# Kernel tuning notes

Measured on AMD Instinct MI355X. Metric: run time of the kernel, lower is better.

The kernel has to match this reference:

```python
import jax, jax.numpy as jnp
import numpy as np

N_NODES = 100000
IN_CH, HIDDEN, OUT_CH = 128, 64, 40
N_EDGES = 1600000


def gcn_conv(x, row, col, W, b, num_nodes):
    """PyG GCNConv: x' = D^-1/2 (A+I) D^-1/2 (x W) + b, self-loops already in row/col."""
    h = x @ W  # [N, out]
    deg = jax.ops.segment_sum(jnp.ones_like(col, dtype=h.dtype), col, num_segments=num_nodes)
    dinv = jnp.where(deg > 0, jax.lax.rsqrt(deg), 0.0)  # [N]
    norm = dinv[row] * dinv[col]  # [E+N]
    msg = h[row] * norm[:, None]  # gather + scale
    out = jax.ops.segment_sum(msg, col, num_segments=num_nodes)  # scatter-add to targets
    return out + b


def setup_inputs() -> dict:
    key = jax.random.key(0)
    k = jax.random.split(key, 6)
    x = jax.random.normal(k[0], (N_NODES, IN_CH), dtype=jnp.float32)
    ei = jax.random.randint(k[1], (2, N_EDGES), 0, N_NODES, dtype=jnp.int64)
    # Glorot-style init for linear weights, zeros for biases (PyG defaults)
    W1 = jax.random.normal(k[2], (IN_CH, HIDDEN), dtype=jnp.float32) / np.sqrt(IN_CH)
    b1 = jnp.zeros((HIDDEN,), dtype=jnp.float32)
    W2 = jax.random.normal(k[3], (HIDDEN, OUT_CH), dtype=jnp.float32) / np.sqrt(HIDDEN)
    b2 = jnp.zeros((OUT_CH,), dtype=jnp.float32)
    return {"x": x, "ei": ei, "W1": W1, "b1": b1, "W2": W2, "b2": b2}


def reference(x, ei, W1, b1, W2, b2):
    num_nodes = x.shape[0]
    loop = jnp.arange(num_nodes, dtype=ei.dtype)
    row = jnp.concatenate([ei[0], loop])  # sources + self-loops
    col = jnp.concatenate([ei[1], loop])  # targets + self-loops
    h = jax.nn.relu(gcn_conv(x, row, col, W1, b1, num_nodes))
    # dropout(p=0.5) is identity in eval mode (deterministic reference)
    return gcn_conv(h, row, col, W2, b2, num_nodes)
```

## Files before the change

### kernel.cpp

```cpp
#include <hip/hip_runtime.h>
#include <hip/hip_bf16.h>
#include <math.h>

#define IN_CH 128
#define HID 64
#define OUT_CH 40
#define NBUCK 1024
#define NBSHIFT 10
#define CAP2 3125
#define CAPL 2560

typedef const __hip_bfloat16* bf16p;
typedef __attribute__((ext_vector_type(8))) short bf16x8;
typedef __attribute__((ext_vector_type(4))) float f32x4;
typedef __attribute__((ext_vector_type(8))) float f32x8;

__device__ __forceinline__ f32x8 cvt8(bf16x8 v) {
    f32x8 o;
    #pragma unroll
    for (int j = 0; j < 8; ++j) {
        unsigned int bits = ((unsigned int)(unsigned short)v[j]) << 16;
        o[j] = __uint_as_float(bits);
    }
    return o;
}

__device__ __forceinline__ bf16x8 pack8(f32x8 v) {
    bf16x8 o;
    #pragma unroll
    for (int j = 0; j < 8; ++j) {
        __hip_bfloat16 b = __float2bfloat16(v[j]);
        o[j] = *reinterpret_cast<short*>(&b);
    }
    return o;
}

__device__ __forceinline__ int bucket_of(int c, int N, float invNB) {
    int b = (int)((float)c * invNB);
    long long cB = (long long)c << NBSHIFT;
    while ((long long)(b + 1) * N <= cB) ++b;
    while (b > 0 && (long long)b * N > cB) --b;
    return b;
}

__global__ __launch_bounds__(256) void k_detectconv(const void* x, const void* ei,
        int* flags, const void* W1, const void* b1, const void* W2, const void* b2,
        float* wf, int* bincnt2) {
    __shared__ int s_f32, s_hi;
    if (threadIdx.x == 0) { s_f32 = 0; s_hi = 0; }
    __syncthreads();
    const __hip_bfloat16* xb = (const __hip_bfloat16*)x;
    const int* ii = (const int*)ei;
    int lf = 0, lh = 0;
    for (int i = threadIdx.x; i < 4096; i += 256) {
        float f = __bfloat162float(xb[i]);
        if (!(fabsf(f) <= 1e4f)) lf = 1;
        lh |= ii[2 * i + 1];
    }
    if (lf) atomicOr(&s_f32, 1);
    if (lh) atomicOr(&s_hi, 1);
    for (int i = threadIdx.x; i < NBUCK; i += 256) bincnt2[i] = 0;
    __syncthreads();
    const int isF32 = s_f32 ? 1 : 0;
    if (threadIdx.x == 0) {
        flags[0] = isF32;
        flags[1] = (s_hi == 0) ? 1 : 0;
        flags[2] = 0;
    }
    for (int i = threadIdx.x; i < 10856; i += 256) {
        const void* src; int off;
        if (i < 8192)       { src = W1; off = i; }
        else if (i < 8256)  { src = b1; off = i - 8192; }
        else if (i < 10816) { src = W2; off = i - 8256; }
        else                { src = b2; off = i - 10816; }
        wf[i] = isF32 ? ((const float*)src)[off]
                      : __bfloat162float(((bf16p)src)[off]);
    }
}

__global__ __launch_bounds__(512) void k_bin2(const int* ei, const int* flags,
        int* bincnt2, long long* bins2, int E, int N, float invNB) {
    __shared__ int cnt[NBUCK], base[NBUCK];
    for (int i = threadIdx.x; i < NBUCK; i += 512) cnt[i] = 0;
    __syncthreads();
    const int i64 = flags[1];
    const int e0 = blockIdx.x * 4096;
    const int e1 = min(e0 + 4096, E);
    int e = e0 + threadIdx.x;
    for (; e + 3 * 512 < e1; e += 4 * 512) {
        int c0 = i64 ? ei[2 * (E + e)]        : ei[E + e];
        int c1 = i64 ? ei[2 * (E + e + 512)]  : ei[E + e + 512];
        int c2 = i64 ? ei[2 * (E + e + 1024)] : ei[E + e + 1024];
        int c3 = i64 ? ei[2 * (E + e + 1536)] : ei[E + e + 1536];
        atomicAdd(&cnt[bucket_of(c0, N, invNB)], 1);
        atomicAdd(&cnt[bucket_of(c1, N, invNB)], 1);
        atomicAdd(&cnt[bucket_of(c2, N, invNB)], 1);
        atomicAdd(&cnt[bucket_of(c3, N, invNB)], 1);
    }
    for (; e < e1; e += 512) {
        int c = i64 ? ei[2 * (E + e)] : ei[E + e];
        atomicAdd(&cnt[bucket_of(c, N, invNB)], 1);
    }
    __syncthreads();
    for (int i = threadIdx.x; i < NBUCK; i += 512) {
        int v = cnt[i];
        base[i] = v ? atomicAdd(&bincnt2[i], v) : 0;
        cnt[i] = 0;
    }
    __syncthreads();
    for (e = e0 + threadIdx.x; e < e1; e += 512) {
        int r, c;
        if (i64) { r = ei[2 * e]; c = ei[2 * (E + e)]; }
        else     { r = ei[e];     c = ei[E + e]; }
        int b = bucket_of(c, N, invNB);
        int slot = base[b] + atomicAdd(&cnt[b], 1);
        if (slot < CAP2)
            bins2[(size_t)b * CAP2 + slot] = ((long long)r << 32) | (unsigned int)c;
    }
}

__global__ __launch_bounds__(256) void k_csr(const long long* bins2, const int* bincnt2,
        int* rowstart, float* dinv, int* erow, int N) {
    __shared__ long long rc[CAPL];
    __shared__ int sdeg[256], lcur[256], red[256];
    const int s = blockIdx.x;
    const int tid = threadIdx.x;
    int part = 0;
    for (int j = tid; j < s; j += 256) part += min(bincnt2[j], CAPL);
    red[tid] = part;
    __syncthreads();
    for (int o = 128; o > 0; o >>= 1) {
        if (tid < o) red[tid] += red[tid + o];
        __syncthreads();
    }
    const int gb = red[0];
    const int nlo = (int)(((long long)s * N + NBUCK - 1) >> NBSHIFT);
    const int nhi = (int)(((long long)(s + 1) * N + NBUCK - 1) >> NBSHIFT);
    const int width = nhi - nlo;
    const int cnt = min(bincnt2[s], CAPL);

    for (int i = tid; i < cnt; i += 256) rc[i] = bins2[(size_t)s * CAP2 + i];
    sdeg[tid] = 0;
    __syncthreads();
    for (int i = tid; i < cnt; i += 256) {
        int j = (int)(rc[i] & 0xffffffffLL) - nlo;
        if (j >= 0 && j < width) atomicAdd(&sdeg[j], 1);
    }
    __syncthreads();
    int my = sdeg[tid];
    __syncthreads();
    for (int off = 1; off < 256; off <<= 1) {
        int t = (tid >= off) ? sdeg[tid - off] : 0;
        __syncthreads();
        sdeg[tid] += t;
        __syncthreads();
    }
    int excl = sdeg[tid] - my;
    lcur[tid] = excl;
    if (tid < width) {
        rowstart[nlo + tid] = gb + excl;
        dinv[nlo + tid] = rsqrtf((float)my + 1.0f);
    }
    if (s == NBUCK - 1 && tid == 0) rowstart[N] = gb + cnt;
    __syncthreads();
    for (int i = tid; i < cnt; i += 256) {
        long long v = rc[i];
        int j = (int)(v & 0xffffffffLL) - nlo;
        if (j >= 0 && j < width) {
            int pos = atomicAdd(&lcur[j], 1);
            erow[gb + pos] = (int)(v >> 32);
        }
    }
}

__global__ __launch_bounds__(256) void k_gemm1_mfma(const void* x, const float* W1f,
        __hip_bfloat16* h1b, const int* flags, int N) {
    __shared__ __align__(16) unsigned short wT[HID][IN_CH];
    for (int i = threadIdx.x; i < IN_CH * HID; i += 256) {
        int k = i >> 6, c = i & 63;
        __hip_bfloat16 b = __float2bfloat16(W1f[i]);
        wT[c][k] = *reinterpret_cast<unsigned short*>(&b);
    }
    __syncthreads();

    const int isF32 = flags[0];
    const int lane = threadIdx.x & 63;
    const int wid  = threadIdx.x >> 6;
    const int r = lane & 15;
    const int g = lane >> 4;

    bf16x8 bfr[4][4];
    #pragma unroll
    for (int nt = 0; nt < 4; ++nt)
        #pragma unroll
        for (int ks = 0; ks < 4; ++ks)
            bfr[nt][ks] = *(const bf16x8*)&wT[nt * 16 + r][ks * 32 + g * 8];

    const int tiles = (N + 15) >> 4;
    for (int t = blockIdx.x * 4 + wid; t < tiles; t += gridDim.x * 4) {
        const int row0 = t * 16;
        int arow = row0 + r; if (arow >= N) arow = N - 1;
        bf16x8 afr[4];
        if (!isF32) {
            const unsigned short* xr = (const unsigned short*)x + (size_t)arow * IN_CH;
            #pragma unroll
            for (int ks = 0; ks < 4; ++ks)
                afr[ks] = *(const bf16x8*)&xr[ks * 32 + g * 8];
        } else {
            const float* xr = (const float*)x + (size_t)arow * IN_CH;
            #pragma unroll
            for (int ks = 0; ks < 4; ++ks) {
                f32x4 a0 = *(const f32x4*)&xr[ks * 32 + g * 8];
                f32x4 a1 = *(const f32x4*)&xr[ks * 32 + g * 8 + 4];
                #pragma unroll
                for (int j = 0; j < 4; ++j) {
                    __hip_bfloat16 b0 = __float2bfloat16(a0[j]);
                    __hip_bfloat16 b1v = __float2bfloat16(a1[j]);
                    afr[ks][j]     = *reinterpret_cast<short*>(&b0);
                    afr[ks][j + 4] = *reinterpret_cast<short*>(&b1v);
                }
            }
        }
        f32x4 acc[4] = {};
        #pragma unroll
        for (int ks = 0; ks < 4; ++ks)
            #pragma unroll
            for (int nt = 0; nt < 4; ++nt)
                acc[nt] = __builtin_amdgcn_mfma_f32_16x16x32_bf16(afr[ks], bfr[nt][ks],
                                                                  acc[nt], 0, 0, 0);
        #pragma unroll
        for (int nt = 0; nt < 4; ++nt) {
            #pragma unroll
            for (int q = 0; q < 4; ++q) {
                int rr = row0 + g * 4 + q;
                if (rr < N)
                    h1b[(size_t)rr * HID + nt * 16 + r] = __float2bfloat16(acc[nt][q]);
            }
        }
    }
}

__global__ __launch_bounds__(256) void k_agg1(const int* rowstart, const int* erow,
        const __hip_bfloat16* h1b, const float* dinv, const float* b1f,
        __hip_bfloat16* g, int N) {
    const int lane = threadIdx.x & 63;
    const int sub = lane >> 3;
    const int co  = lane & 7;
    const f32x4 b1a = *(const f32x4*)&b1f[co * 8];
    const f32x4 b1b = *(const f32x4*)&b1f[co * 8 + 4];
    const int wstride = (gridDim.x * 256) >> 6;
    for (int w = (blockIdx.x * 256 + threadIdx.x) >> 6; w < N; w += wstride) {
        int s0 = __builtin_amdgcn_readfirstlane(rowstart[w]);
        int s1 = __builtin_amdgcn_readfirstlane(rowstart[w + 1]);
        float d = dinv[w];
        bf16x8 sv = *(const bf16x8*)&h1b[(size_t)w * HID + co * 8];
        f32x8 acc = {};
        int i = s0 + sub;
        for (; i + 8 < s1; i += 16) {
            int r0 = erow[i], r1 = erow[i + 8];
            float n0 = dinv[r0] * d, n1 = dinv[r1] * d;
            f32x8 v0 = cvt8(*(const bf16x8*)&h1b[(size_t)r0 * HID + co * 8]);
            f32x8 v1 = cvt8(*(const bf16x8*)&h1b[(size_t)r1 * HID + co * 8]);
            #pragma unroll
            for (int j = 0; j < 8; ++j) {
                acc[j] = fmaf(v0[j], n0, acc[j]);
                acc[j] = fmaf(v1[j], n1, acc[j]);
            }
        }
        if (i < s1) {
            int r0 = erow[i];
            float n0 = dinv[r0] * d;
            f32x8 v0 = cvt8(*(const bf16x8*)&h1b[(size_t)r0 * HID + co * 8]);
            #pragma unroll
            for (int j = 0; j < 8; ++j) acc[j] = fmaf(v0[j], n0, acc[j]);
        }
        #pragma unroll
        for (int j = 0; j < 8; ++j) {
            acc[j] += __shfl_xor(acc[j], 8);
            acc[j] += __shfl_xor(acc[j], 16);
            acc[j] += __shfl_xor(acc[j], 32);
        }
        if (sub == 0) {
            float dd = d * d;
            f32x8 sf = cvt8(sv);
            f32x8 gv;
            #pragma unroll
            for (int j = 0; j < 4; ++j) {
                gv[j]     = fmaxf(fmaf(sf[j], dd, acc[j]) + b1a[j], 0.f);
                gv[j + 4] = fmaxf(fmaf(sf[j + 4], dd, acc[j + 4]) + b1b[j], 0.f);
            }
            *(bf16x8*)&g[(size_t)w * HID + co * 8] = pack8(gv);
        }
    }
}

__global__ __launch_bounds__(256) void k_agg2s(const int* rowstart, const int* erow,
        const __hip_bfloat16* g, const float* dinv, __hip_bfloat16* sbuf, int N) {
    const int lane = threadIdx.x & 63;
    const int sub = lane >> 3;
    const int co  = lane & 7;
    const int wstride = (gridDim.x * 256) >> 6;
    for (int w = (blockIdx.x * 256 + threadIdx.x) >> 6; w < N; w += wstride) {
        int s0 = __builtin_amdgcn_readfirstlane(rowstart[w]);
        int s1 = __builtin_amdgcn_readfirstlane(rowstart[w + 1]);
        float d = dinv[w];
        bf16x8 sv = *(const bf16x8*)&g[(size_t)w * HID + co * 8];
        f32x8 acc = {};
        int i = s0 + sub;
        for (; i + 8 < s1; i += 16) {
            int r0 = erow[i], r1 = erow[i + 8];
            float n0 = dinv[r0] * d, n1 = dinv[r1] * d;
            f32x8 v0 = cvt8(*(const bf16x8*)&g[(size_t)r0 * HID + co * 8]);
            f32x8 v1 = cvt8(*(const bf16x8*)&g[(size_t)r1 * HID + co * 8]);
            #pragma unroll
            for (int j = 0; j < 8; ++j) {
                acc[j] = fmaf(v0[j], n0, acc[j]);
                acc[j] = fmaf(v1[j], n1, acc[j]);
            }
        }
        if (i < s1) {
            int r0 = erow[i];
            float n0 = dinv[r0] * d;
            f32x8 v0 = cvt8(*(const bf16x8*)&g[(size_t)r0 * HID + co * 8]);
            #pragma unroll
            for (int j = 0; j < 8; ++j) acc[j] = fmaf(v0[j], n0, acc[j]);
        }
        #pragma unroll
        for (int j = 0; j < 8; ++j) {
            acc[j] += __shfl_xor(acc[j], 8);
            acc[j] += __shfl_xor(acc[j], 16);
            acc[j] += __shfl_xor(acc[j], 32);
        }
        if (sub == 0) {
            float dd = d * d;
            f32x8 sf = cvt8(sv);
            f32x8 ov;
            #pragma unroll
            for (int j = 0; j < 8; ++j) ov[j] = fmaf(sf[j], dd, acc[j]);
            *(bf16x8*)&sbuf[(size_t)w * HID + co * 8] = pack8(ov);
        }
    }
}

__global__ __launch_bounds__(256) void k_gemm2_mfma(const __hip_bfloat16* sbuf,
        const float* W2f, const float* b2f, float* out, int N) {
    __shared__ __align__(16) unsigned short w2T[48][HID];
    for (int i = threadIdx.x; i < 48 * HID; i += 256) {
        int c = i >> 6, k = i & 63;
        float v = (c < OUT_CH) ? W2f[k * OUT_CH + c] : 0.f;
        __hip_bfloat16 b = __float2bfloat16(v);
        w2T[c][k] = *reinterpret_cast<unsigned short*>(&b);
    }
    __syncthreads();

    const int lane = threadIdx.x & 63;
    const int wid  = threadIdx.x >> 6;
    const int r = lane & 15;
    const int gq = lane >> 4;

    bf16x8 bfr[3][2];
    #pragma unroll
    for (int nt = 0; nt < 3; ++nt)
        #pragma unroll
        for (int ks = 0; ks < 2; ++ks)
            bfr[nt][ks] = *(const bf16x8*)&w2T[nt * 16 + r][ks * 32 + gq * 8];
    float b2v[3];
    #pragma unroll
    for (int nt = 0; nt < 3; ++nt)
        b2v[nt] = (nt * 16 + r < OUT_CH) ? b2f[nt * 16 + r] : 0.f;

    const int tiles = (N + 15) >> 4;
    for (int t = blockIdx.x * 4 + wid; t < tiles; t += gridDim.x * 4) {
        const int row0 = t * 16;
        int arow = row0 + r; if (arow >= N) arow = N - 1;
        const unsigned short* sr = (const unsigned short*)sbuf + (size_t)arow * HID;
        bf16x8 afr[2];
        afr[0] = *(const bf16x8*)&sr[gq * 8];
        afr[1] = *(const bf16x8*)&sr[32 + gq * 8];
        f32x4 acc[3] = {};
        #pragma unroll
        for (int ks = 0; ks < 2; ++ks)
            #pragma unroll
            for (int nt = 0; nt < 3; ++nt)
                acc[nt] = __builtin_amdgcn_mfma_f32_16x16x32_bf16(afr[ks], bfr[nt][ks],
                                                                  acc[nt], 0, 0, 0);
        #pragma unroll
        for (int nt = 0; nt < 3; ++nt) {
            int c = nt * 16 + r;
            #pragma unroll
            for (int q = 0; q < 4; ++q) {
                int rr = row0 + gq * 4 + q;
                if (rr < N && c < OUT_CH)
                    out[(size_t)rr * OUT_CH + c] = acc[nt][q] + b2v[nt];
            }
        }
    }
}

extern "C" void kernel_launch(void* const* d_in, const int* in_sizes, int n_in,
                              void* d_out, int out_size, void* d_ws, size_t ws_size,
                              hipStream_t stream) {
    const void* x  = d_in[0];
    const void* ei = d_in[1];
    const void* W1 = d_in[2];
    const void* b1 = d_in[3];
    const void* W2 = d_in[4];
    const void* b2 = d_in[5];
    const int N = in_sizes[0] / IN_CH;
    const int E = in_sizes[1] / 2;
    const int* eii = (const int*)ei;

    float* ws = (float*)d_ws;
    size_t off = 16;
    int*   flags    = (int*)ws;
    int*   bincnt2  = (int*)ws + off;            off += NBUCK;
    float* dinv     = ws + off;                  off += N;
    float* wf       = ws + off;                  off += 10880;
    int*   rowstart = (int*)ws + off;            off += N + 1;
    off = (off + 255) & ~(size_t)255;
    int*   erow     = (int*)ws + off;            off += E;
    off = (off + 255) & ~(size_t)255;
    __hip_bfloat16* h1b = (__hip_bfloat16*)(ws + off);     off += (size_t)N * HID / 2;
    __hip_bfloat16* g   = (__hip_bfloat16*)(ws + off);     off += (size_t)N * HID / 2;
    __hip_bfloat16* sbuf = h1b;
    long long* bins2 = (long long*)h1b;

    k_detectconv<<<1, 256, 0, stream>>>(x, ei, flags, W1, b1, W2, b2, wf, bincnt2);

    float invNB = (float)NBUCK / (float)N;
    int nbin = (E + 4095) / 4096;
    k_bin2<<<nbin, 512, 0, stream>>>(eii, flags, bincnt2, bins2, E, N, invNB);
    k_csr<<<NBUCK, 256, 0, stream>>>(bins2, bincnt2, rowstart, dinv, erow, N);

    int tiles = (N + 15) / 16;
    int g1 = (tiles + 7) / 8;
    k_gemm1_mfma<<<g1, 256, 0, stream>>>(x, wf, h1b, flags, N);

    k_agg1<<<4096, 256, 0, stream>>>(rowstart, erow, h1b, dinv, wf + 8192, g, N);
    k_agg2s<<<4096, 256, 0, stream>>>(rowstart, erow, g, dinv, sbuf, N);
    k_gemm2_mfma<<<g1, 256, 0, stream>>>(sbuf, wf + 8256, wf + 10816, (float*)d_out, N);
}
```

Baseline: 270.9 us.

## Pre-scale features by dinv and pack edge bins into 32-bit words

The symmetric normalization is folded into the features. GEMM1 output is multiplied by dinv[src], and the layer-1 output is multiplied by dinv again before storage, so both aggregation kernels become plain sums with no per-edge dinv gather or multiply. The edge bins also shrink from 64-bit (row,col) pairs to 32-bit words holding the row shifted left by 7 and the column offset within the bucket, which halves binning traffic and shared memory in k_csr. The packing assumes node ids fit in 25 bits and bucket widths are at most 128, and pre-scaling rounds to bf16 at a different point.

```diff
diff --git a/kernel.cpp b/kernel.cpp
--- a/kernel.cpp
+++ b/kernel.cpp
@@ -79,7 +79,7 @@
 }
 
 __global__ __launch_bounds__(512) void k_bin2(const int* ei, const int* flags,
-        int* bincnt2, long long* bins2, int E, int N, float invNB) {
+        int* bincnt2, unsigned int* bins2, int E, int N, float invNB) {
     __shared__ int cnt[NBUCK], base[NBUCK];
     for (int i = threadIdx.x; i < NBUCK; i += 512) cnt[i] = 0;
     __syncthreads();
@@ -113,15 +113,17 @@
         if (i64) { r = ei[2 * e]; c = ei[2 * (E + e)]; }
         else     { r = ei[e];     c = ei[E + e]; }
         int b = bucket_of(c, N, invNB);
+        int nlo = (int)(((long long)b * N + NBUCK - 1) >> NBSHIFT);
         int slot = base[b] + atomicAdd(&cnt[b], 1);
         if (slot < CAP2)
-            bins2[(size_t)b * CAP2 + slot] = ((long long)r << 32) | (unsigned int)c;
-    }
-}
-
-__global__ __launch_bounds__(256) void k_csr(const long long* bins2, const int* bincnt2,
+            bins2[(size_t)b * CAP2 + slot] =
+                ((unsigned int)r << 7) | (unsigned int)(c - nlo);
+    }
+}
+
+__global__ __launch_bounds__(256) void k_csr(const unsigned int* bins2, const int* bincnt2,
         int* rowstart, float* dinv, int* erow, int N) {
-    __shared__ long long rc[CAPL];
+    __shared__ unsigned int rc[CAPL];
     __shared__ int sdeg[256], lcur[256], red[256];
     const int s = blockIdx.x;
     const int tid = threadIdx.x;
@@ -143,8 +145,8 @@
     sdeg[tid] = 0;
     __syncthreads();
     for (int i = tid; i < cnt; i += 256) {
-        int j = (int)(rc[i] & 0xffffffffLL) - nlo;
-        if (j >= 0 && j < width) atomicAdd(&sdeg[j], 1);
+        int j = (int)(rc[i] & 127u);
+        if (j < width) atomicAdd(&sdeg[j], 1);
     }
     __syncthreads();
     int my = sdeg[tid];
@@ -164,17 +166,17 @@
     if (s == NBUCK - 1 && tid == 0) rowstart[N] = gb + cnt;
     __syncthreads();
     for (int i = tid; i < cnt; i += 256) {
-        long long v = rc[i];
-        int j = (int)(v & 0xffffffffLL) - nlo;
-        if (j >= 0 && j < width) {
+        unsigned int v = rc[i];
+        int j = (int)(v & 127u);
+        if (j < width) {
             int pos = atomicAdd(&lcur[j], 1);
-            erow[gb + pos] = (int)(v >> 32);
+            erow[gb + pos] = (int)(v >> 7);
         }
     }
 }
 
 __global__ __launch_bounds__(256) void k_gemm1_mfma(const void* x, const float* W1f,
-        __hip_bfloat16* h1b, const int* flags, int N) {
+        const float* dinv, __hip_bfloat16* h1s, const int* flags, int N) {
     __shared__ __align__(16) unsigned short wT[HID][IN_CH];
     for (int i = threadIdx.x; i < IN_CH * HID; i += 256) {
         int k = i >> 6, c = i & 63;
@@ -229,20 +231,22 @@
                 acc[nt] = __builtin_amdgcn_mfma_f32_16x16x32_bf16(afr[ks], bfr[nt][ks],
                                                                   acc[nt], 0, 0, 0);
         #pragma unroll
-        for (int nt = 0; nt < 4; ++nt) {
-            #pragma unroll
-            for (int q = 0; q < 4; ++q) {
-                int rr = row0 + g * 4 + q;
-                if (rr < N)
-                    h1b[(size_t)rr * HID + nt * 16 + r] = __float2bfloat16(acc[nt][q]);
+        for (int q = 0; q < 4; ++q) {
+            int rr = row0 + g * 4 + q;
+            if (rr < N) {
+                float dv = dinv[rr];
+                #pragma unroll
+                for (int nt = 0; nt < 4; ++nt)
+                    h1s[(size_t)rr * HID + nt * 16 + r] =
+                        __float2bfloat16(acc[nt][q] * dv);
             }
         }
     }
 }
 
 __global__ __launch_bounds__(256) void k_agg1(const int* rowstart, const int* erow,
-        const __hip_bfloat16* h1b, const float* dinv, const float* b1f,
-        __hip_bfloat16* g, int N) {
+        const __hip_bfloat16* h1s, const float* dinv, const float* b1f,
+        __hip_bfloat16* gs, int N) {
     const int lane = threadIdx.x & 63;
     const int sub = lane >> 3;
     const int co  = lane & 7;
@@ -253,26 +257,21 @@
         int s0 = __builtin_amdgcn_readfirstlane(rowstart[w]);
         int s1 = __builtin_amdgcn_readfirstlane(rowstart[w + 1]);
         float d = dinv[w];
-        bf16x8 sv = *(const bf16x8*)&h1b[(size_t)w * HID + co * 8];
+        bf16x8 sv = *(const bf16x8*)&h1s[(size_t)w * HID + co * 8];
         f32x8 acc = {};
         int i = s0 + sub;
         for (; i + 8 < s1; i += 16) {
             int r0 = erow[i], r1 = erow[i + 8];
-            float n0 = dinv[r0] * d, n1 = dinv[r1] * d;
-            f32x8 v0 = cvt8(*(const bf16x8*)&h1b[(size_t)r0 * HID + co * 8]);
-            f32x8 v1 = cvt8(*(const bf16x8*)&h1b[(size_t)r1 * HID + co * 8]);
-            #pragma unroll
-            for (int j = 0; j < 8; ++j) {
-                acc[j] = fmaf(v0[j], n0, acc[j]);
-                acc[j] = fmaf(v1[j], n1, acc[j]);
-            }
+            f32x8 v0 = cvt8(*(const bf16x8*)&h1s[(size_t)r0 * HID + co * 8]);
+            f32x8 v1 = cvt8(*(const bf16x8*)&h1s[(size_t)r1 * HID + co * 8]);
+            #pragma unroll
+            for (int j = 0; j < 8; ++j) acc[j] += v0[j] + v1[j];
         }
         if (i < s1) {
             int r0 = erow[i];
-            float n0 = dinv[r0] * d;
-            f32x8 v0 = cvt8(*(const bf16x8*)&h1b[(size_t)r0 * HID + co * 8]);
-            #pragma unroll
-            for (int j = 0; j < 8; ++j) acc[j] = fmaf(v0[j], n0, acc[j]);
+            f32x8 v0 = cvt8(*(const bf16x8*)&h1s[(size_t)r0 * HID + co * 8]);
+            #pragma unroll
+            for (int j = 0; j < 8; ++j) acc[j] += v0[j];
         }
         #pragma unroll
         for (int j = 0; j < 8; ++j) {
@@ -281,21 +280,22 @@
             acc[j] += __shfl_xor(acc[j], 32);
         }
         if (sub == 0) {
-            float dd = d * d;
             f32x8 sf = cvt8(sv);
             f32x8 gv;
             #pragma unroll
             for (int j = 0; j < 4; ++j) {
-                gv[j]     = fmaxf(fmaf(sf[j], dd, acc[j]) + b1a[j], 0.f);
-                gv[j + 4] = fmaxf(fmaf(sf[j + 4], dd, acc[j + 4]) + b1b[j], 0.f);
+                float ga = fmaxf(fmaf(d, sf[j] + acc[j], b1a[j]), 0.f);
+                float gb = fmaxf(fmaf(d, sf[j + 4] + acc[j + 4], b1b[j]), 0.f);
+                gv[j]     = ga * d;
+                gv[j + 4] = gb * d;
             }
-            *(bf16x8*)&g[(size_t)w * HID + co * 8] = pack8(gv);
+            *(bf16x8*)&gs[(size_t)w * HID + co * 8] = pack8(gv);
         }
     }
 }
 
 __global__ __launch_bounds__(256) void k_agg2s(const int* rowstart, const int* erow,
-        const __hip_bfloat16* g, const float* dinv, __hip_bfloat16* sbuf, int N) {
+        const __hip_bfloat16* gs, const float* dinv, __hip_bfloat16* sbuf, int N) {
     const int lane = threadIdx.x & 63;
     const int sub = lane >> 3;
     const int co  = lane & 7;
@@ -304,26 +304,21 @@
         int s0 = __builtin_amdgcn_readfirstlane(rowstart[w]);
         int s1 = __builtin_amdgcn_readfirstlane(rowstart[w + 1]);
         float d = dinv[w];
-        bf16x8 sv = *(const bf16x8*)&g[(size_t)w * HID + co * 8];
+        bf16x8 sv = *(const bf16x8*)&gs[(size_t)w * HID + co * 8];
         f32x8 acc = {};
         int i = s0 + sub;
         for (; i + 8 < s1; i += 16) {
             int r0 = erow[i], r1 = erow[i + 8];
-            float n0 = dinv[r0] * d, n1 = dinv[r1] * d;
-            f32x8 v0 = cvt8(*(const bf16x8*)&g[(size_t)r0 * HID + co * 8]);
-            f32x8 v1 = cvt8(*(const bf16x8*)&g[(size_t)r1 * HID + co * 8]);
-            #pragma unroll
-            for (int j = 0; j < 8; ++j) {
-                acc[j] = fmaf(v0[j], n0, acc[j]);
-                acc[j] = fmaf(v1[j], n1, acc[j]);
-            }
+            f32x8 v0 = cvt8(*(const bf16x8*)&gs[(size_t)r0 * HID + co * 8]);
+            f32x8 v1 = cvt8(*(const bf16x8*)&gs[(size_t)r1 * HID + co * 8]);
+            #pragma unroll
+            for (int j = 0; j < 8; ++j) acc[j] += v0[j] + v1[j];
         }
         if (i < s1) {
             int r0 = erow[i];
-            float n0 = dinv[r0] * d;
-            f32x8 v0 = cvt8(*(const bf16x8*)&g[(size_t)r0 * HID + co * 8]);
-            #pragma unroll
-            for (int j = 0; j < 8; ++j) acc[j] = fmaf(v0[j], n0, acc[j]);
+            f32x8 v0 = cvt8(*(const bf16x8*)&gs[(size_t)r0 * HID + co * 8]);
+            #pragma unroll
+            for (int j = 0; j < 8; ++j) acc[j] += v0[j];
         }
         #pragma unroll
         for (int j = 0; j < 8; ++j) {
@@ -332,11 +327,10 @@
             acc[j] += __shfl_xor(acc[j], 32);
         }
         if (sub == 0) {
-            float dd = d * d;
             f32x8 sf = cvt8(sv);
             f32x8 ov;
             #pragma unroll
-            for (int j = 0; j < 8; ++j) ov[j] = fmaf(sf[j], dd, acc[j]);
+            for (int j = 0; j < 8; ++j) ov[j] = d * (sf[j] + acc[j]);
             *(bf16x8*)&sbuf[(size_t)w * HID + co * 8] = pack8(ov);
         }
     }
@@ -420,10 +414,10 @@
     off = (off + 255) & ~(size_t)255;
     int*   erow     = (int*)ws + off;            off += E;
     off = (off + 255) & ~(size_t)255;
-    __hip_bfloat16* h1b = (__hip_bfloat16*)(ws + off);     off += (size_t)N * HID / 2;
-    __hip_bfloat16* g   = (__hip_bfloat16*)(ws + off);     off += (size_t)N * HID / 2;
-    __hip_bfloat16* sbuf = h1b;
-    long long* bins2 = (long long*)h1b;
+    __hip_bfloat16* h1s = (__hip_bfloat16*)(ws + off);     off += (size_t)N * HID / 2;
+    __hip_bfloat16* gsb = (__hip_bfloat16*)(ws + off);     off += (size_t)N * HID / 2;
+    __hip_bfloat16* sbuf = h1s;
+    unsigned int* bins2 = (unsigned int*)h1s;
 
     k_detectconv<<<1, 256, 0, stream>>>(x, ei, flags, W1, b1, W2, b2, wf, bincnt2);
 
@@ -434,9 +428,9 @@
 
     int tiles = (N + 15) / 16;
     int g1 = (tiles + 7) / 8;
-    k_gemm1_mfma<<<g1, 256, 0, stream>>>(x, wf, h1b, flags, N);
-
-    k_agg1<<<4096, 256, 0, stream>>>(rowstart, erow, h1b, dinv, wf + 8192, g, N);
-    k_agg2s<<<4096, 256, 0, stream>>>(rowstart, erow, g, dinv, sbuf, N);
+    k_gemm1_mfma<<<g1, 256, 0, stream>>>(x, wf, dinv, h1s, flags, N);
+
+    k_agg1<<<4096, 256, 0, stream>>>(rowstart, erow, h1s, dinv, wf + 8192, gsb, N);
+    k_agg2s<<<4096, 256, 0, stream>>>(rowstart, erow, gsb, dinv, sbuf, N);
     k_gemm2_mfma<<<g1, 256, 0, stream>>>(sbuf, wf + 8256, wf + 10816, (float*)d_out, N);
 }
```

New measurement: 261.1 us. -3.7%, faster.
